# Kernel tuning notes

Measured on AMD Instinct MI355X. Metric: run time of the kernel, lower is better.

Reference implementation:

```python
import jax, jax.numpy as jnp
import numpy as np

D = 256       # video_dim == gcn_dims == interaction_dim
FD = 512      # forward_dim = 2 * interaction_dim
UPDATE_RATE = 0.5


def setup_inputs() -> dict:
    key = jax.random.key(0)
    ks = jax.random.split(key, 20)
    T, N = 768, 384
    s = lambda *sh: 1.0 / np.sqrt(sh[-1])
    return {
        "video_features": jax.random.normal(ks[0], (T, D), jnp.float32),
        "text_features": jax.random.normal(ks[1], (N, D), jnp.float32),
        "video_position_embedding": jax.random.normal(ks[2], (T, D), jnp.float32),
        "text_position_embedding": jax.random.normal(ks[3], (N, D), jnp.float32),
        # VideoEncoder conv1d (out=D, in=D, k=3)
        "conv_w": jax.random.normal(ks[4], (D, D, 3), jnp.float32) * (1.0 / np.sqrt(D * 3)),
        "conv_b": jax.random.normal(ks[5], (D,), jnp.float32) * 0.01,
        # TextGnnEncoder
        "bil_w": jax.random.normal(ks[6], (D, D), jnp.float32) * s(D, D),
        "lin_w": jax.random.normal(ks[7], (D, D), jnp.float32) * s(D, D),
        "lin_b": jax.random.normal(ks[8], (D,), jnp.float32) * 0.01,
        # PairInteraction
        "W1": jax.random.normal(ks[9], (FD, D), jnp.float32) * s(FD, D),
        "b1": jax.random.normal(ks[10], (FD,), jnp.float32) * 0.01,
        "W2": jax.random.normal(ks[11], (FD, D), jnp.float32) * s(FD, D),
        "Wi": jax.random.normal(ks[12], (D, FD), jnp.float32) * s(D, FD),
        "bi": jax.random.normal(ks[13], (D,), jnp.float32) * 0.01,
        # amplifier generators (Linear(interaction_dim, 1))
        "wt": jax.random.normal(ks[14], (D,), jnp.float32) * s(D,),
        "bt": jax.random.normal(ks[15], (1,), jnp.float32) * 0.01,
        "wv": jax.random.normal(ks[16], (D,), jnp.float32) * s(D,),
        "bv": jax.random.normal(ks[17], (1,), jnp.float32) * 0.01,
    }


def _forward(video_features, text_features, video_position_embedding, text_position_embedding,
             conv_w, conv_b, bil_w, lin_w, lin_b, W1, b1, W2, Wi, bi, wt, bt, wv, bv):
    T, N = video_features.shape[0], text_features.shape[0]
    input_video, input_text = video_features, text_features

    v = video_features + video_position_embedding          # (T, D)
    t = text_features + text_position_embedding            # (N, D)

    # VideoEncoder: Conv1d(k=3, pad=1) over time, then ReLU (dropout=0 in eval)
    x = v.T[None]                                           # (1, D, T)
    x = jax.lax.conv_general_dilated(x, conv_w, (1,), [(1, 1)],
                                     dimension_numbers=("NCH", "OIH", "NCH"))
    v = jax.nn.relu(x[0] + conv_b[:, None]).T               # (T, D)

    # TextGnnEncoder
    tn = t / jnp.maximum(jnp.linalg.norm(t, axis=1, keepdims=True), 1e-12)  # L2 normalize rows
    edges = (tn @ bil_w.T) @ tn.T                            # (N, N)
    weights = jax.nn.sigmoid(jnp.mean(edges, axis=1, keepdims=True))        # (N, 1)
    t = weights * (tn @ lin_w.T + lin_b)                     # (N, D)

    # PairInteraction: broadcast add + ReLU + Linear
    f1 = v @ W1.T + b1                                       # (T, FD)
    f2 = t @ W2.T                                            # (N, FD)
    h = jax.nn.relu(f1[:, None, :] + f2[None, :, :])         # (T, N, FD)
    imap = jnp.einsum("tnf,of->tno", h, Wi) + bi             # (T, N, D)

    # dual softmax attention pooling
    text_att = jax.nn.softmax(imap @ wt + bt, axis=1)        # (T, N), softmax over N
    text_context = jnp.einsum("tn,nd->td", text_att, t)      # (T, D)
    video_att = jax.nn.softmax(imap @ wv + bv, axis=0)       # (T, N), softmax over T
    video_context = jnp.einsum("tn,td->nd", video_att, v)    # (N, D)

    ur = UPDATE_RATE
    t_out = video_context * ur + t * (1.0 - ur) + input_text
    v_out = text_context * ur + v * (1.0 - ur) + input_video
    return v_out, t_out


def reference(video_features, text_features, video_position_embedding, text_position_embedding,
              conv_w, conv_b, bil_w, lin_w, lin_b, W1, b1, W2, Wi, bi, wt, bt, wv, bv):
    return _forward(video_features, text_features, video_position_embedding, text_position_embedding,
                    conv_w, conv_b, bil_w, lin_w, lin_b, W1, b1, W2, Wi, bi, wt, bt, wv, bv)
```

## Files before the change

### kernel.cpp

```cpp
#include <hip/hip_runtime.h>
#include <math.h>

#define D  256
#define T  768
#define N  384
#define FD 512

#define DOT4(A,B) ((A).x*(B).x + (A).y*(B).y + (A).z*(B).z + (A).w*(B).w)

__global__ __launch_bounds__(256) void k_front(
    const float* __restrict__ vf, const float* __restrict__ vpos,
    const float* __restrict__ cw,
    const float* __restrict__ tf, const float* __restrict__ tpos,
    const float* __restrict__ lin_w, const float* __restrict__ lin_b,
    const float* __restrict__ Wi, const float* __restrict__ wt,
    const float* __restrict__ wv,
    float* __restrict__ vep, float* __restrict__ tn,
    float* __restrict__ tl, float* __restrict__ ut, float* __restrict__ uv)
{
    __shared__ float smem[10880];
    const int b = blockIdx.x, tid = threadIdx.x;

    if (b < 288) {
        const int k  = b % 3;
        const int rem = b / 3;
        const int t0 = (rem % 12) * 64;
        const int o0 = (rem / 12) * 32;
        float (*As)[68] = (float(*)[68])smem;
        float (*Bs)[68] = (float(*)[68])(smem + 4352);
        const int p = tid >> 4, oi = tid & 15;
        float a00=0.f,a01=0.f,a10=0.f,a11=0.f,a20=0.f,a21=0.f,a30=0.f,a31=0.f;

        for (int c = 0; c < 4; ++c) {
            const int i0 = c << 6;
            __syncthreads();
#pragma unroll
            for (int s = 0; s < 4; ++s) {
                int u = tid + (s << 8);
                int r = u >> 4, q4 = (u & 15) * 4;
                int gr = t0 + r + k - 1;
                float4 v = make_float4(0.f,0.f,0.f,0.f);
                if (gr >= 0 && gr < T) {
                    float4 x = *(const float4*)&vf[gr*D + i0 + q4];
                    float4 y = *(const float4*)&vpos[gr*D + i0 + q4];
                    v = make_float4(x.x+y.x, x.y+y.y, x.z+y.z, x.w+y.w);
                }
                *(float4*)&As[r][q4] = v;
            }
#pragma unroll
            for (int s = 0; s < 8; ++s) {
                int u = tid + (s << 8);
                int o = u >> 6, i = u & 63;
                Bs[o][i] = cw[(o0 + o)*768 + (i0 + i)*3 + k];
            }
            __syncthreads();
#pragma unroll 4
            for (int kc4 = 0; kc4 < 16; ++kc4) {
                float4 r0 = *(const float4*)&As[4*p    ][kc4*4];
                float4 r1 = *(const float4*)&As[4*p + 1][kc4*4];
                float4 r2 = *(const float4*)&As[4*p + 2][kc4*4];
                float4 r3 = *(const float4*)&As[4*p + 3][kc4*4];
                float4 b0 = *(const float4*)&Bs[oi     ][kc4*4];
                float4 b1 = *(const float4*)&Bs[oi + 16][kc4*4];
                a00 += DOT4(r0,b0); a01 += DOT4(r0,b1);
                a10 += DOT4(r1,b0); a11 += DOT4(r1,b1);
                a20 += DOT4(r2,b0); a21 += DOT4(r2,b1);
                a30 += DOT4(r3,b0); a31 += DOT4(r3,b1);
            }
        }
        float* vz = vep + k * (T*D);
        const int t = t0 + 4*p;
        vz[(t  )*D + o0 + oi] = a00;  vz[(t  )*D + o0 + oi + 16] = a01;
        vz[(t+1)*D + o0 + oi] = a10;  vz[(t+1)*D + o0 + oi + 16] = a11;
        vz[(t+2)*D + o0 + oi] = a20;  vz[(t+2)*D + o0 + oi + 16] = a21;
        vz[(t+3)*D + o0 + oi] = a30;  vz[(t+3)*D + o0 + oi + 16] = a31;
    } else if (b < 384) {
        const int wid = tid >> 6, lane = tid & 63;
        const int r = (b - 288)*4 + wid;
        float v[4]; float ss = 0.f;
#pragma unroll
        for (int kk = 0; kk < 4; ++kk) {
            v[kk] = tf[r*D + lane + 64*kk] + tpos[r*D + lane + 64*kk];
            ss += v[kk]*v[kk];
        }
#pragma unroll
        for (int off = 1; off < 64; off <<= 1) ss += __shfl_xor(ss, off);
        float inv = 1.0f / fmaxf(sqrtf(ss), 1e-12f);
#pragma unroll
        for (int kk = 0; kk < 4; ++kk) tn[r*D + lane + 64*kk] = v[kk] * inv;
    } else if (b < 480) {
        const int bb = b - 384;
        const int n0 = (bb >> 3) * 32;
        const int o0 = (bb & 7) * 32;
        float (*As2)[260] = (float(*)[260])smem;
        float (*Bs2)[68]  = (float(*)[68])(smem + 8320);
        float* inv = smem + 10496;
#pragma unroll
        for (int s = 0; s < 8; ++s) {
            int u = tid + (s << 8);
            int r = u >> 6, q4 = (u & 63) * 4;
            float4 x = *(const float4*)&tf[(n0 + r)*D + q4];
            float4 y = *(const float4*)&tpos[(n0 + r)*D + q4];
            *(float4*)&As2[r][q4] = make_float4(x.x+y.x, x.y+y.y, x.z+y.z, x.w+y.w);
        }
        __syncthreads();
        {
            const int r = tid >> 3, j = tid & 7;
            float p = 0.f;
#pragma unroll
            for (int m = 0; m < 8; ++m) {
                float4 a = *(const float4*)&As2[r][j*32 + m*4];
                p += DOT4(a, a);
            }
            p += __shfl_xor(p, 1); p += __shfl_xor(p, 2); p += __shfl_xor(p, 4);
            if (j == 0) inv[r] = 1.0f / fmaxf(sqrtf(p), 1e-12f);
        }
        const int tA = tid >> 4, oA = tid & 15;
        float acc00=0.f, acc01=0.f, acc10=0.f, acc11=0.f;
        for (int c = 0; c < 4; ++c) {
            const int d0 = c << 6;
            __syncthreads();
#pragma unroll
            for (int s = 0; s < 2; ++s) {
                int u = tid + (s << 8);
                int o = u >> 4, q4 = (u & 15) * 4;
                *(float4*)&Bs2[o][q4] = *(const float4*)&lin_w[(o0 + o)*D + d0 + q4];
            }
            __syncthreads();
#pragma unroll 4
            for (int kc4 = 0; kc4 < 16; ++kc4) {
                float4 a0 = *(const float4*)&As2[tA     ][d0 + kc4*4];
                float4 a1 = *(const float4*)&As2[tA + 16][d0 + kc4*4];
                float4 b0 = *(const float4*)&Bs2[oA     ][kc4*4];
                float4 b1 = *(const float4*)&Bs2[oA + 16][kc4*4];
                acc00 += DOT4(a0,b0); acc01 += DOT4(a0,b1);
                acc10 += DOT4(a1,b0); acc11 += DOT4(a1,b1);
            }
        }
        const float i0n = inv[tA], i1n = inv[tA + 16];
        const float lb0 = lin_b[o0 + oA], lb1 = lin_b[o0 + oA + 16];
        tl[(n0 + tA     )*D + o0 + oA]      = i0n*acc00 + lb0;
        tl[(n0 + tA     )*D + o0 + oA + 16] = i0n*acc01 + lb1;
        tl[(n0 + tA + 16)*D + o0 + oA]      = i1n*acc10 + lb0;
        tl[(n0 + tA + 16)*D + o0 + oA + 16] = i1n*acc11 + lb1;
    } else {
        float* wsm = smem;
        const int which = b - 480;
        const float* w = (which < 2) ? wt : wv;
        float* u = (which < 2) ? ut : uv;
        const int f = ((which & 1) << 8) + tid;
        wsm[tid] = w[tid];
        __syncthreads();
        float s = 0.f;
#pragma unroll 4
        for (int d = 0; d < D; ++d) s += wsm[d] * Wi[d*FD + f];
        u[f] = s;
    }
}

__global__ __launch_bounds__(256) void k_mid(
    const float* __restrict__ vep, const float* __restrict__ cbp,
    const float* __restrict__ W1, const float* __restrict__ b1v,
    const float* __restrict__ tlp, const float* __restrict__ W2,
    const float* __restrict__ tn, const float* __restrict__ bil,
    float* __restrict__ f1, float* __restrict__ f2,
    float* __restrict__ ve, float* __restrict__ q)
{
    __shared__ float smem[6656];
    const int b = blockIdx.x, tid = threadIdx.x;

    if (b < 288) {
        const bool isF1 = (b < 192);
        const int bb = isF1 ? b : b - 192;
        const int nT = isF1 ? 12 : 6;
        const int r0 = (bb % nT) * 64;
        const int f0 = (bb / nT) * 32;
        float (*As)[68] = (float(*)[68])smem;
        float (*Bs)[68] = (float(*)[68])(smem + 4352);
        const int p = tid >> 4, fi = tid & 15;
        float a00=0.f,a01=0.f,a10=0.f,a11=0.f,a20=0.f,a21=0.f,a30=0.f,a31=0.f;
        const float* Wp = isF1 ? W1 : W2;

        for (int c = 0; c < 4; ++c) {
            const int d0 = c << 6;
            __syncthreads();
            if (isF1) {
#pragma unroll
                for (int s = 0; s < 4; ++s) {
                    int u = tid + (s << 8);
                    int r = u >> 4, q4 = (u & 15) * 4;
                    const int off = (r0 + r)*D + d0 + q4;
                    float4 p0 = *(const float4*)&vep[off];
                    float4 p1 = *(const float4*)&vep[T*D + off];
                    float4 p2 = *(const float4*)&vep[2*T*D + off];
                    float4 cbv = *(const float4*)&cbp[d0 + q4];
                    float4 v;
                    v.x = fmaxf(p0.x+p1.x+p2.x+cbv.x, 0.f);
                    v.y = fmaxf(p0.y+p1.y+p2.y+cbv.y, 0.f);
                    v.z = fmaxf(p0.z+p1.z+p2.z+cbv.z, 0.f);
                    v.w = fmaxf(p0.w+p1.w+p2.w+cbv.w, 0.f);
                    *(float4*)&As[r][q4] = v;
                }
            } else {
#pragma unroll
                for (int s = 0; s < 4; ++s) {
                    int u = tid + (s << 8);
                    int r = u >> 4, q4 = (u & 15) * 4;
                    *(float4*)&As[r][q4] = *(const float4*)&tlp[(r0 + r)*D + d0 + q4];
                }
            }
#pragma unroll
            for (int s = 0; s < 2; ++s) {
                int u = tid + (s << 8);
                int o = u >> 4, q4 = (u & 15) * 4;
                *(float4*)&Bs[o][q4] = *(const float4*)&Wp[(f0 + o)*D + d0 + q4];
            }
            __syncthreads();
#pragma unroll 4
            for (int kc4 = 0; kc4 < 16; ++kc4) {
                float4 r0v = *(const float4*)&As[4*p    ][kc4*4];
                float4 r1v = *(const float4*)&As[4*p + 1][kc4*4];
                float4 r2v = *(const float4*)&As[4*p + 2][kc4*4];
                float4 r3v = *(const float4*)&As[4*p + 3][kc4*4];
                float4 b0 = *(const float4*)&Bs[fi     ][kc4*4];
                float4 b1 = *(const float4*)&Bs[fi + 16][kc4*4];
                a00 += DOT4(r0v,b0); a01 += DOT4(r0v,b1);
                a10 += DOT4(r1v,b0); a11 += DOT4(r1v,b1);
                a20 += DOT4(r2v,b0); a21 += DOT4(r2v,b1);
                a30 += DOT4(r3v,b0); a31 += DOT4(r3v,b1);
            }
        }
        const int r = r0 + 4*p;
        if (isF1) {
            const float bi0 = b1v[f0 + fi], bi1 = b1v[f0 + fi + 16];
            f1[(r  )*FD + f0 + fi] = a00 + bi0;  f1[(r  )*FD + f0 + fi + 16] = a01 + bi1;
            f1[(r+1)*FD + f0 + fi] = a10 + bi0;  f1[(r+1)*FD + f0 + fi + 16] = a11 + bi1;
            f1[(r+2)*FD + f0 + fi] = a20 + bi0;  f1[(r+2)*FD + f0 + fi + 16] = a21 + bi1;
            f1[(r+3)*FD + f0 + fi] = a30 + bi0;  f1[(r+3)*FD + f0 + fi + 16] = a31 + bi1;
        } else {
            f2[(r  )*FD + f0 + fi] = a00;  f2[(r  )*FD + f0 + fi + 16] = a01;
            f2[(r+1)*FD + f0 + fi] = a10;  f2[(r+1)*FD + f0 + fi + 16] = a11;
            f2[(r+2)*FD + f0 + fi] = a20;  f2[(r+2)*FD + f0 + fi + 16] = a21;
            f2[(r+3)*FD + f0 + fi] = a30;  f2[(r+3)*FD + f0 + fi + 16] = a31;
        }
    } else if (b < 384) {
        const int t0 = (b - 288) * 8;
        float cbv = cbp[tid];
#pragma unroll
        for (int r = 0; r < 8; ++r) {
            const int off = (t0 + r)*D + tid;
            float s = vep[off] + vep[T*D + off] + vep[2*T*D + off] + cbv;
            ve[off] = fmaxf(s, 0.f);
        }
    } else {
        float* tb = smem;
        float (*qp)[32] = (float(*)[32])(smem + 256);
        const int bq = b - 384;
        float s = 0.f;
#pragma unroll 8
        for (int n = 0; n < N; ++n) s += tn[n*D + tid];
        tb[tid] = s * (1.0f / (float)N);
        __syncthreads();
        const int o = tid & 31, dg = tid >> 5;
        float p = 0.f;
#pragma unroll 8
        for (int d = dg*32; d < dg*32 + 32; ++d) p += tb[d] * bil[d*D + bq*32 + o];
        qp[dg][o] = p;
        __syncthreads();
        if (tid < 32) {
            float acc = 0.f;
#pragma unroll
            for (int kk = 0; kk < 8; ++kk) acc += qp[kk][tid];
            q[bq*32 + tid] = acc;
        }
    }
}

__global__ __launch_bounds__(256) void k_score(
    const float* __restrict__ f1, const float* __restrict__ f2,
    const float* __restrict__ tn, const float* __restrict__ qv,
    const float* __restrict__ tlp,
    const float* __restrict__ ut, const float* __restrict__ uv,
    float* __restrict__ stp, float* __restrict__ svp, float* __restrict__ tg)
{
    __shared__ float smem[9216];
    const int tid = threadIdx.x;
    const int bid = blockIdx.x;

    if (bid < 576) {
        const int t0 = (bid % 12) * 64;
        const int n0 = ((bid / 12) % 6) * 64;
        const int iz = bid / 72;
        const int fz = iz * 64;
        float (*f1s)[68] = (float(*)[68])smem;
        float (*f2s)[68] = (float(*)[68])(smem + 4352);
        float* qs   = smem + 8704;
        float* us_t = smem + 8960;
        float* us_v = smem + 9024;
        float* wsm  = smem + 9088;

        qs[tid] = qv[tid];
        if (tid < 64) us_t[tid] = ut[fz + tid];
        else if (tid < 128) us_v[tid - 64] = uv[fz + tid - 64];
        __syncthreads();
        {
            const int r = tid >> 2, j = tid & 3;
            float p = 0.f;
#pragma unroll
            for (int m = 0; m < 16; ++m) {
                float4 a = *(const float4*)&tn[(n0 + r)*D + j*64 + m*4];
                float4 qq = *(const float4*)&qs[j*64 + m*4];
                p += DOT4(a, qq);
            }
            p += __shfl_xor(p, 1); p += __shfl_xor(p, 2);
            if (j == 0) wsm[r] = 1.0f / (1.0f + expf(-p));
        }
#pragma unroll
        for (int s = 0; s < 4; ++s) {
            int u = tid + (s << 8);
            int r = u >> 4, q4 = (u & 15) * 4;
            *(float4*)&f1s[r][q4] = *(const float4*)&f1[(t0 + r)*FD + fz + q4];
        }
        __syncthreads();
#pragma unroll
        for (int s = 0; s < 4; ++s) {
            int u = tid + (s << 8);
            int r = u >> 4, q4 = (u & 15) * 4;
            float w = wsm[r];
            float4 v = *(const float4*)&f2[(n0 + r)*FD + fz + q4];
            *(float4*)&f2s[r][q4] = make_float4(w*v.x, w*v.y, w*v.z, w*v.w);
        }
        __syncthreads();

        const int ti = tid >> 4, ni = tid & 15;
        float at[4][4], av[4][4];
#pragma unroll
        for (int i = 0; i < 4; ++i)
#pragma unroll
            for (int j = 0; j < 4; ++j) { at[i][j] = 0.f; av[i][j] = 0.f; }

#pragma unroll 2
        for (int fq = 0; fq < 16; ++fq) {
            float a[4][4], bb[4][4], utv[4], uvv[4];
            *(float4*)utv  = *(const float4*)&us_t[fq*4];
            *(float4*)uvv  = *(const float4*)&us_v[fq*4];
#pragma unroll
            for (int i = 0; i < 4; ++i) {
                *(float4*)a[i]  = *(const float4*)&f1s[ti + 16*i][fq*4];
                *(float4*)bb[i] = *(const float4*)&f2s[ni + 16*i][fq*4];
            }
#pragma unroll
            for (int e = 0; e < 4; ++e) {
#pragma unroll
                for (int i = 0; i < 4; ++i) {
#pragma unroll
                    for (int j = 0; j < 4; ++j) {
                        float h = fmaxf(a[i][e] + bb[j][e], 0.f);
                        at[i][j] += h * utv[e];
                        av[i][j] += h * uvv[e];
                    }
                }
            }
        }
        float* stz = stp + iz * (T*N);
        float* svz = svp + iz * (N*T);
#pragma unroll
        for (int i = 0; i < 4; ++i) {
            const int t = t0 + ti + 16*i;
#pragma unroll
            for (int j = 0; j < 4; ++j) {
                const int n = n0 + ni + 16*j;
                stz[t*N + n] = at[i][j];
                svz[n*T + t] = av[i][j];
            }
        }
    } else {
        const int n0 = (bid - 576) * 32;
        float* qs  = smem;
        float* wsm = smem + 256;
        qs[tid] = qv[tid];
        __syncthreads();
        {
            const int r = tid >> 3, j = tid & 7;
            float p = 0.f;
#pragma unroll
            for (int m = 0; m < 8; ++m) {
                float4 a = *(const float4*)&tn[(n0 + r)*D + j*32 + m*4];
                float4 qq = *(const float4*)&qs[j*32 + m*4];
                p += DOT4(a, qq);
            }
            p += __shfl_xor(p, 1); p += __shfl_xor(p, 2); p += __shfl_xor(p, 4);
            if (j == 0) wsm[r] = 1.0f / (1.0f + expf(-p));
        }
        __syncthreads();
#pragma unroll
        for (int r = 0; r < 32; ++r)
            tg[(n0 + r)*D + tid] = wsm[r] * tlp[(n0 + r)*D + tid];
    }
}

__global__ __launch_bounds__(256) void k_att(
    const float* __restrict__ stp, const float* __restrict__ svp,
    const float* __restrict__ tg, const float* __restrict__ ve,
    const float* __restrict__ vf, const float* __restrict__ tf,
    float* __restrict__ out_v, float* __restrict__ out_t)
{
    __shared__ float attb[768][4];
    __shared__ float red[4][4];
    __shared__ float ptA[4][4][64];
    __shared__ float ptB[4][4][64];
    const int tid = threadIdx.x;
    const int oo = tid & 63, g = tid >> 6;
    const int TN = T*N;

    if (blockIdx.x < 384) {
        const int bx = blockIdx.x >> 1, h = blockIdx.x & 1;
        const int t0 = bx * 4;
        const int oA = h*128 + oo, oB = oA + 64;

        float v1[4], v2[4];
#pragma unroll
        for (int r = 0; r < 4; ++r) {
            const float* p = stp + (t0 + r)*N + tid;
            float s1 = 0.f;
#pragma unroll
            for (int z = 0; z < 8; ++z) s1 += p[z*TN];
            v1[r] = s1;
            if (tid < 128) {
                float s2 = 0.f;
#pragma unroll
                for (int z = 0; z < 8; ++z) s2 += p[z*TN + 256];
                v2[r] = s2;
            } else v2[r] = -1e30f;
        }
        float m[4], si[4];
#pragma unroll
        for (int r = 0; r < 4; ++r) {
            float mm = fmaxf(v1[r], v2[r]);
#pragma unroll
            for (int off = 1; off < 64; off <<= 1) mm = fmaxf(mm, __shfl_xor(mm, off));
            if (oo == 0) red[g][r] = mm;
        }
        __syncthreads();
#pragma unroll
        for (int r = 0; r < 4; ++r)
            m[r] = fmaxf(fmaxf(red[0][r], red[1][r]), fmaxf(red[2][r], red[3][r]));
        __syncthreads();
        float e1[4], e2[4];
#pragma unroll
        for (int r = 0; r < 4; ++r) {
            e1[r] = expf(v1[r] - m[r]);
            e2[r] = (tid < 128) ? expf(v2[r] - m[r]) : 0.f;
            float ss = e1[r] + e2[r];
#pragma unroll
            for (int off = 1; off < 64; off <<= 1) ss += __shfl_xor(ss, off);
            if (oo == 0) red[g][r] = ss;
        }
        __syncthreads();
#pragma unroll
        for (int r = 0; r < 4; ++r)
            si[r] = 1.0f / (red[0][r] + red[1][r] + red[2][r] + red[3][r]);
#pragma unroll
        for (int r = 0; r < 4; ++r) {
            attb[tid][r] = e1[r] * si[r];
            if (tid < 128) attb[tid + 256][r] = e2[r] * si[r];
        }
        __syncthreads();

        float accA[4] = {0.f,0.f,0.f,0.f};
        float accB[4] = {0.f,0.f,0.f,0.f};
#pragma unroll 4
        for (int n = g; n < N; n += 4) {
            float4 a0 = *(const float4*)&attb[n][0];
            float tvA = tg[n*D + oA], tvB = tg[n*D + oB];
            accA[0] += a0.x*tvA; accA[1] += a0.y*tvA; accA[2] += a0.z*tvA; accA[3] += a0.w*tvA;
            accB[0] += a0.x*tvB; accB[1] += a0.y*tvB; accB[2] += a0.z*tvB; accB[3] += a0.w*tvB;
        }
#pragma unroll
        for (int r = 0; r < 4; ++r) { ptA[g][r][oo] = accA[r]; ptB[g][r][oo] = accB[r]; }
        __syncthreads();
        if (g < 4) {
            const int rr = g;
            float sA = ptA[0][rr][oo] + ptA[1][rr][oo] + ptA[2][rr][oo] + ptA[3][rr][oo];
            float sB = ptB[0][rr][oo] + ptB[1][rr][oo] + ptB[2][rr][oo] + ptB[3][rr][oo];
            int t = t0 + rr;
            out_v[t*D + oA] = 0.5f*sA + 0.5f*ve[t*D + oA] + vf[t*D + oA];
            out_v[t*D + oB] = 0.5f*sB + 0.5f*ve[t*D + oB] + vf[t*D + oB];
        }
    } else {
        const int b2 = blockIdx.x - 384;
        const int bx = b2 >> 1, h = b2 & 1;
        const int n0 = bx * 4;
        const int oA = h*128 + oo, oB = oA + 64;

        float v1[4], v2[4], v3[4];
#pragma unroll
        for (int r = 0; r < 4; ++r) {
            const float* p = svp + (n0 + r)*T + tid;
            float s1 = 0.f, s2 = 0.f, s3 = 0.f;
#pragma unroll
            for (int z = 0; z < 8; ++z) {
                s1 += p[z*TN];
                s2 += p[z*TN + 256];
                s3 += p[z*TN + 512];
            }
            v1[r] = s1; v2[r] = s2; v3[r] = s3;
        }
        float m[4], si[4];
#pragma unroll
        for (int r = 0; r < 4; ++r) {
            float mm = fmaxf(fmaxf(v1[r], v2[r]), v3[r]);
#pragma unroll
            for (int off = 1; off < 64; off <<= 1) mm = fmaxf(mm, __shfl_xor(mm, off));
            if (oo == 0) red[g][r] = mm;
        }
        __syncthreads();
#pragma unroll
        for (int r = 0; r < 4; ++r)
            m[r] = fmaxf(fmaxf(red[0][r], red[1][r]), fmaxf(red[2][r], red[3][r]));
        __syncthreads();
        float e1[4], e2[4], e3[4];
#pragma unroll
        for (int r = 0; r < 4; ++r) {
            e1[r] = expf(v1[r] - m[r]);
            e2[r] = expf(v2[r] - m[r]);
            e3[r] = expf(v3[r] - m[r]);
            float ss = e1[r] + e2[r] + e3[r];
#pragma unroll
            for (int off = 1; off < 64; off <<= 1) ss += __shfl_xor(ss, off);
            if (oo == 0) red[g][r] = ss;
        }
        __syncthreads();
#pragma unroll
        for (int r = 0; r < 4; ++r)
            si[r] = 1.0f / (red[0][r] + red[1][r] + red[2][r] + red[3][r]);
#pragma unroll
        for (int r = 0; r < 4; ++r) {
            attb[tid][r]       = e1[r] * si[r];
            attb[tid + 256][r] = e2[r] * si[r];
            attb[tid + 512][r] = e3[r] * si[r];
        }
        __syncthreads();

        float accA[4] = {0.f,0.f,0.f,0.f};
        float accB[4] = {0.f,0.f,0.f,0.f};
#pragma unroll 4
        for (int t = g; t < T; t += 4) {
            float4 a0 = *(const float4*)&attb[t][0];
            float vvA = ve[t*D + oA], vvB = ve[t*D + oB];
            accA[0] += a0.x*vvA; accA[1] += a0.y*vvA; accA[2] += a0.z*vvA; accA[3] += a0.w*vvA;
            accB[0] += a0.x*vvB; accB[1] += a0.y*vvB; accB[2] += a0.z*vvB; accB[3] += a0.w*vvB;
        }
#pragma unroll
        for (int r = 0; r < 4; ++r) { ptA[g][r][oo] = accA[r]; ptB[g][r][oo] = accB[r]; }
        __syncthreads();
        if (g < 4) {
            const int rr = g;
            float sA = ptA[0][rr][oo] + ptA[1][rr][oo] + ptA[2][rr][oo] + ptA[3][rr][oo];
            float sB = ptB[0][rr][oo] + ptB[1][rr][oo] + ptB[2][rr][oo] + ptB[3][rr][oo];
            int n = n0 + rr;
            out_t[n*D + oA] = 0.5f*sA + 0.5f*tg[n*D + oA] + tf[n*D + oA];
            out_t[n*D + oB] = 0.5f*sB + 0.5f*tg[n*D + oB] + tf[n*D + oB];
        }
    }
}

extern "C" void kernel_launch(void* const* d_in, const int* in_sizes, int n_in,
                              void* d_out, int out_size, void* d_ws, size_t ws_size,
                              hipStream_t stream)
{
    (void)in_sizes; (void)n_in; (void)out_size; (void)ws_size;
    const float* vf   = (const float*)d_in[0];
    const float* tf   = (const float*)d_in[1];
    const float* vpos = (const float*)d_in[2];
    const float* tpos = (const float*)d_in[3];
    const float* cw   = (const float*)d_in[4];
    const float* cb   = (const float*)d_in[5];
    const float* bil  = (const float*)d_in[6];
    const float* lw   = (const float*)d_in[7];
    const float* lb   = (const float*)d_in[8];
    const float* W1   = (const float*)d_in[9];
    const float* b1   = (const float*)d_in[10];
    const float* W2   = (const float*)d_in[11];
    const float* Wi   = (const float*)d_in[12];
    const float* wt   = (const float*)d_in[14];
    const float* wv   = (const float*)d_in[16];

    float* ws  = (float*)d_ws;
    float* vep = ws;
    float* ve  = vep + 3*T*D;
    float* tn  = ve + T*D;
    float* tl  = tn + N*D;
    float* tg  = tl + N*D;
    float* f1  = tg + N*D;
    float* f2  = f1 + T*FD;
    float* q   = f2 + N*FD;
    float* ut  = q + D;
    float* uv  = ut + FD;
    float* stp = uv + FD;
    float* svp = stp + 8*T*N;

    float* out_v = (float*)d_out;
    float* out_t = out_v + T*D;

    hipLaunchKernelGGL(k_front, dim3(484), dim3(256), 0, stream,
                       vf, vpos, cw, tf, tpos, lw, lb, Wi, wt, wv, vep, tn, tl, ut, uv);
    hipLaunchKernelGGL(k_mid,   dim3(392), dim3(256), 0, stream,
                       vep, cb, W1, b1, tl, W2, tn, bil, f1, f2, ve, q);
    hipLaunchKernelGGL(k_score, dim3(588), dim3(256), 0, stream,
                       f1, f2, tn, q, tl, ut, uv, stp, svp, tg);
    hipLaunchKernelGGL(k_att,   dim3(576), dim3(256), 0, stream,
                       stp, svp, tg, ve, vf, tf, out_v, out_t);
}
```

Baseline: 99.22 us.

## Retile score kernel to 32x32 with fewer F-splits and coalesced stores; widen attention rows

The score kernel now uses 32x32 (t,n) tiles with the F dimension split two ways instead of eight, looping over four 64-wide F chunks inside the block. This cuts the partial-score buffers from 8 to 2 and so reduces the traffic that the attention kernel must read and sum. Results are staged through shared memory so both the row-major and transposed partial outputs are written as coalesced float4 stores. The attention kernel processes 8 rows per block instead of 4, halving its grid and reusing each loaded tg/ve value across more rows. In exchange each thread carries a smaller 2x2 register tile with less ILP, and both kernels now do more serial work per block on fewer blocks.

```diff
diff --git a/kernel.cpp b/kernel.cpp
--- a/kernel.cpp
+++ b/kernel.cpp
@@ -283,96 +283,93 @@
     const float* __restrict__ ut, const float* __restrict__ uv,
     float* __restrict__ stp, float* __restrict__ svp, float* __restrict__ tg)
 {
-    __shared__ float smem[9216];
+    __shared__ float smem[5152];
     const int tid = threadIdx.x;
     const int bid = blockIdx.x;
 
     if (bid < 576) {
-        const int t0 = (bid % 12) * 64;
-        const int n0 = ((bid / 12) % 6) * 64;
-        const int iz = bid / 72;
-        const int fz = iz * 64;
+        const int t0 = (bid % 24) * 32;
+        const int n0 = ((bid / 24) % 12) * 32;
+        const int iz = bid / 288;
+        const int fh = iz * 256;
         float (*f1s)[68] = (float(*)[68])smem;
-        float (*f2s)[68] = (float(*)[68])(smem + 4352);
-        float* qs   = smem + 8704;
-        float* us_t = smem + 8960;
-        float* us_v = smem + 9024;
-        float* wsm  = smem + 9088;
-
-        qs[tid] = qv[tid];
-        if (tid < 64) us_t[tid] = ut[fz + tid];
-        else if (tid < 128) us_v[tid - 64] = uv[fz + tid - 64];
+        float (*f2s)[68] = (float(*)[68])(smem + 2176);
+        float* us_t = smem + 4352;
+        float* us_v = smem + 4608;
+        float* qs   = smem + 4864;
+        float* wsm  = smem + 5120;
+
+        qs[tid]   = qv[tid];
+        us_t[tid] = ut[fh + tid];
+        us_v[tid] = uv[fh + tid];
         __syncthreads();
         {
-            const int r = tid >> 2, j = tid & 3;
+            const int r = tid >> 3, j = tid & 7;
             float p = 0.f;
 #pragma unroll
-            for (int m = 0; m < 16; ++m) {
-                float4 a = *(const float4*)&tn[(n0 + r)*D + j*64 + m*4];
-                float4 qq = *(const float4*)&qs[j*64 + m*4];
+            for (int m = 0; m < 8; ++m) {
+                float4 a = *(const float4*)&tn[(n0 + r)*D + j*32 + m*4];
+                float4 qq = *(const float4*)&qs[j*32 + m*4];
                 p += DOT4(a, qq);
             }
-            p += __shfl_xor(p, 1); p += __shfl_xor(p, 2);
+            p += __shfl_xor(p, 1); p += __shfl_xor(p, 2); p += __shfl_xor(p, 4);
             if (j == 0) wsm[r] = 1.0f / (1.0f + expf(-p));
         }
-#pragma unroll
-        for (int s = 0; s < 4; ++s) {
-            int u = tid + (s << 8);
-            int r = u >> 4, q4 = (u & 15) * 4;
-            *(float4*)&f1s[r][q4] = *(const float4*)&f1[(t0 + r)*FD + fz + q4];
-        }
-        __syncthreads();
-#pragma unroll
-        for (int s = 0; s < 4; ++s) {
-            int u = tid + (s << 8);
-            int r = u >> 4, q4 = (u & 15) * 4;
-            float w = wsm[r];
-            float4 v = *(const float4*)&f2[(n0 + r)*FD + fz + q4];
-            *(float4*)&f2s[r][q4] = make_float4(w*v.x, w*v.y, w*v.z, w*v.w);
-        }
-        __syncthreads();
 
         const int ti = tid >> 4, ni = tid & 15;
-        float at[4][4], av[4][4];
-#pragma unroll
-        for (int i = 0; i < 4; ++i)
-#pragma unroll
-            for (int j = 0; j < 4; ++j) { at[i][j] = 0.f; av[i][j] = 0.f; }
-
-#pragma unroll 2
-        for (int fq = 0; fq < 16; ++fq) {
-            float a[4][4], bb[4][4], utv[4], uvv[4];
-            *(float4*)utv  = *(const float4*)&us_t[fq*4];
-            *(float4*)uvv  = *(const float4*)&us_v[fq*4];
-#pragma unroll
-            for (int i = 0; i < 4; ++i) {
-                *(float4*)a[i]  = *(const float4*)&f1s[ti + 16*i][fq*4];
-                *(float4*)bb[i] = *(const float4*)&f2s[ni + 16*i][fq*4];
-            }
-#pragma unroll
-            for (int e = 0; e < 4; ++e) {
-#pragma unroll
-                for (int i = 0; i < 4; ++i) {
-#pragma unroll
-                    for (int j = 0; j < 4; ++j) {
-                        float h = fmaxf(a[i][e] + bb[j][e], 0.f);
-                        at[i][j] += h * utv[e];
-                        av[i][j] += h * uvv[e];
-                    }
+        float at[2][2] = {{0.f,0.f},{0.f,0.f}};
+        float av[2][2] = {{0.f,0.f},{0.f,0.f}};
+
+        for (int c = 0; c < 4; ++c) {
+            const int f00 = fh + c*64;
+            __syncthreads();
+#pragma unroll
+            for (int s = 0; s < 2; ++s) {
+                int u = tid + (s << 8);
+                int r = u >> 4, q4 = (u & 15) * 4;
+                *(float4*)&f1s[r][q4] = *(const float4*)&f1[(t0 + r)*FD + f00 + q4];
+                float w = wsm[r];
+                float4 v = *(const float4*)&f2[(n0 + r)*FD + f00 + q4];
+                *(float4*)&f2s[r][q4] = make_float4(w*v.x, w*v.y, w*v.z, w*v.w);
+            }
+            __syncthreads();
+#pragma unroll 4
+            for (int fq = 0; fq < 16; ++fq) {
+                float utv[4], uvv[4], a0[4], a1[4], b0[4], b1[4];
+                *(float4*)utv = *(const float4*)&us_t[c*64 + fq*4];
+                *(float4*)uvv = *(const float4*)&us_v[c*64 + fq*4];
+                *(float4*)a0  = *(const float4*)&f1s[ti     ][fq*4];
+                *(float4*)a1  = *(const float4*)&f1s[ti + 16][fq*4];
+                *(float4*)b0  = *(const float4*)&f2s[ni     ][fq*4];
+                *(float4*)b1  = *(const float4*)&f2s[ni + 16][fq*4];
+#pragma unroll
+                for (int e = 0; e < 4; ++e) {
+                    float h00 = fmaxf(a0[e] + b0[e], 0.f);
+                    float h01 = fmaxf(a0[e] + b1[e], 0.f);
+                    float h10 = fmaxf(a1[e] + b0[e], 0.f);
+                    float h11 = fmaxf(a1[e] + b1[e], 0.f);
+                    at[0][0] += h00*utv[e]; av[0][0] += h00*uvv[e];
+                    at[0][1] += h01*utv[e]; av[0][1] += h01*uvv[e];
+                    at[1][0] += h10*utv[e]; av[1][0] += h10*uvv[e];
+                    at[1][1] += h11*utv[e]; av[1][1] += h11*uvv[e];
                 }
             }
         }
+        __syncthreads();
+#pragma unroll
+        for (int i = 0; i < 2; ++i)
+#pragma unroll
+            for (int j = 0; j < 2; ++j) {
+                f1s[ti + 16*i][ni + 16*j] = at[i][j];
+                f2s[ni + 16*j][ti + 16*i] = av[i][j];
+            }
+        __syncthreads();
         float* stz = stp + iz * (T*N);
         float* svz = svp + iz * (N*T);
-#pragma unroll
-        for (int i = 0; i < 4; ++i) {
-            const int t = t0 + ti + 16*i;
-#pragma unroll
-            for (int j = 0; j < 4; ++j) {
-                const int n = n0 + ni + 16*j;
-                stz[t*N + n] = at[i][j];
-                svz[n*T + t] = av[i][j];
-            }
+        {
+            const int row = tid >> 3, c4 = (tid & 7) * 4;
+            *(float4*)&stz[(t0 + row)*N + n0 + c4] = *(const float4*)&f1s[row][c4];
+            *(float4*)&svz[(n0 + row)*T + t0 + c4] = *(const float4*)&f2s[row][c4];
         }
     } else {
         const int n0 = (bid - 576) * 32;
@@ -405,37 +402,29 @@
     const float* __restrict__ vf, const float* __restrict__ tf,
     float* __restrict__ out_v, float* __restrict__ out_t)
 {
-    __shared__ float attb[768][4];
-    __shared__ float red[4][4];
-    __shared__ float ptA[4][4][64];
-    __shared__ float ptB[4][4][64];
+    __shared__ float attb[768][8];
+    __shared__ float red[4][8];
+    __shared__ float ptA[4][8][64];
+    __shared__ float ptB[4][8][64];
     const int tid = threadIdx.x;
     const int oo = tid & 63, g = tid >> 6;
     const int TN = T*N;
 
-    if (blockIdx.x < 384) {
+    if (blockIdx.x < 192) {
         const int bx = blockIdx.x >> 1, h = blockIdx.x & 1;
-        const int t0 = bx * 4;
+        const int t0 = bx * 8;
         const int oA = h*128 + oo, oB = oA + 64;
 
-        float v1[4], v2[4];
-#pragma unroll
-        for (int r = 0; r < 4; ++r) {
+        float v1[8], v2[8];
+#pragma unroll
+        for (int r = 0; r < 8; ++r) {
             const float* p = stp + (t0 + r)*N + tid;
-            float s1 = 0.f;
-#pragma unroll
-            for (int z = 0; z < 8; ++z) s1 += p[z*TN];
-            v1[r] = s1;
-            if (tid < 128) {
-                float s2 = 0.f;
-#pragma unroll
-                for (int z = 0; z < 8; ++z) s2 += p[z*TN + 256];
-                v2[r] = s2;
-            } else v2[r] = -1e30f;
-        }
-        float m[4], si[4];
-#pragma unroll
-        for (int r = 0; r < 4; ++r) {
+            v1[r] = p[0] + p[TN];
+            v2[r] = (tid < 128) ? (p[256] + p[TN + 256]) : -1e30f;
+        }
+        float m[8], si[8];
+#pragma unroll
+        for (int r = 0; r < 8; ++r) {
             float mm = fmaxf(v1[r], v2[r]);
 #pragma unroll
             for (int off = 1; off < 64; off <<= 1) mm = fmaxf(mm, __shfl_xor(mm, off));
@@ -443,12 +432,12 @@
         }
         __syncthreads();
 #pragma unroll
-        for (int r = 0; r < 4; ++r)
+        for (int r = 0; r < 8; ++r)
             m[r] = fmaxf(fmaxf(red[0][r], red[1][r]), fmaxf(red[2][r], red[3][r]));
         __syncthreads();
-        float e1[4], e2[4];
-#pragma unroll
-        for (int r = 0; r < 4; ++r) {
+        float e1[8], e2[8];
+#pragma unroll
+        for (int r = 0; r < 8; ++r) {
             e1[r] = expf(v1[r] - m[r]);
             e2[r] = (tid < 128) ? expf(v2[r] - m[r]) : 0.f;
             float ss = e1[r] + e2[r];
@@ -458,29 +447,32 @@
         }
         __syncthreads();
 #pragma unroll
-        for (int r = 0; r < 4; ++r)
+        for (int r = 0; r < 8; ++r)
             si[r] = 1.0f / (red[0][r] + red[1][r] + red[2][r] + red[3][r]);
 #pragma unroll
-        for (int r = 0; r < 4; ++r) {
+        for (int r = 0; r < 8; ++r) {
             attb[tid][r] = e1[r] * si[r];
             if (tid < 128) attb[tid + 256][r] = e2[r] * si[r];
         }
         __syncthreads();
 
-        float accA[4] = {0.f,0.f,0.f,0.f};
-        float accB[4] = {0.f,0.f,0.f,0.f};
+        float accA[8] = {0.f,0.f,0.f,0.f,0.f,0.f,0.f,0.f};
+        float accB[8] = {0.f,0.f,0.f,0.f,0.f,0.f,0.f,0.f};
 #pragma unroll 4
         for (int n = g; n < N; n += 4) {
             float4 a0 = *(const float4*)&attb[n][0];
+            float4 a1 = *(const float4*)&attb[n][4];
             float tvA = tg[n*D + oA], tvB = tg[n*D + oB];
             accA[0] += a0.x*tvA; accA[1] += a0.y*tvA; accA[2] += a0.z*tvA; accA[3] += a0.w*tvA;
+            accA[4] += a1.x*tvA; accA[5] += a1.y*tvA; accA[6] += a1.z*tvA; accA[7] += a1.w*tvA;
             accB[0] += a0.x*tvB; accB[1] += a0.y*tvB; accB[2] += a0.z*tvB; accB[3] += a0.w*tvB;
-        }
-#pragma unroll
-        for (int r = 0; r < 4; ++r) { ptA[g][r][oo] = accA[r]; ptB[g][r][oo] = accB[r]; }
-        __syncthreads();
-        if (g < 4) {
-            const int rr = g;
+            accB[4] += a1.x*tvB; accB[5] += a1.y*tvB; accB[6] += a1.z*tvB; accB[7] += a1.w*tvB;
+        }
+#pragma unroll
+        for (int r = 0; r < 8; ++r) { ptA[g][r][oo] = accA[r]; ptB[g][r][oo] = accB[r]; }
+        __syncthreads();
+#pragma unroll
+        for (int rr = g; rr < 8; rr += 4) {
             float sA = ptA[0][rr][oo] + ptA[1][rr][oo] + ptA[2][rr][oo] + ptA[3][rr][oo];
             float sB = ptB[0][rr][oo] + ptB[1][rr][oo] + ptB[2][rr][oo] + ptB[3][rr][oo];
             int t = t0 + rr;
@@ -488,27 +480,22 @@
             out_v[t*D + oB] = 0.5f*sB + 0.5f*ve[t*D + oB] + vf[t*D + oB];
         }
     } else {
-        const int b2 = blockIdx.x - 384;
+        const int b2 = blockIdx.x - 192;
         const int bx = b2 >> 1, h = b2 & 1;
-        const int n0 = bx * 4;
+        const int n0 = bx * 8;
         const int oA = h*128 + oo, oB = oA + 64;
 
-        float v1[4], v2[4], v3[4];
-#pragma unroll
-        for (int r = 0; r < 4; ++r) {
+        float v1[8], v2[8], v3[8];
+#pragma unroll
+        for (int r = 0; r < 8; ++r) {
             const float* p = svp + (n0 + r)*T + tid;
-            float s1 = 0.f, s2 = 0.f, s3 = 0.f;
-#pragma unroll
-            for (int z = 0; z < 8; ++z) {
-                s1 += p[z*TN];
-                s2 += p[z*TN + 256];
-                s3 += p[z*TN + 512];
-            }
-            v1[r] = s1; v2[r] = s2; v3[r] = s3;
-        }
-        float m[4], si[4];
-#pragma unroll
-        for (int r = 0; r < 4; ++r) {
+            v1[r] = p[0]   + p[TN];
+            v2[r] = p[256] + p[TN + 256];
+            v3[r] = p[512] + p[TN + 512];
+        }
+        float m[8], si[8];
+#pragma unroll
+        for (int r = 0; r < 8; ++r) {
             float mm = fmaxf(fmaxf(v1[r], v2[r]), v3[r]);
 #pragma unroll
             for (int off = 1; off < 64; off <<= 1) mm = fmaxf(mm, __shfl_xor(mm, off));
@@ -516,12 +503,12 @@
         }
         __syncthreads();
 #pragma unroll
-        for (int r = 0; r < 4; ++r)
+        for (int r = 0; r < 8; ++r)
             m[r] = fmaxf(fmaxf(red[0][r], red[1][r]), fmaxf(red[2][r], red[3][r]));
         __syncthreads();
-        float e1[4], e2[4], e3[4];
-#pragma unroll
-        for (int r = 0; r < 4; ++r) {
+        float e1[8], e2[8], e3[8];
+#pragma unroll
+        for (int r = 0; r < 8; ++r) {
             e1[r] = expf(v1[r] - m[r]);
             e2[r] = expf(v2[r] - m[r]);
             e3[r] = expf(v3[r] - m[r]);
@@ -532,30 +519,33 @@
         }
         __syncthreads();
 #pragma unroll
-        for (int r = 0; r < 4; ++r)
+        for (int r = 0; r < 8; ++r)
             si[r] = 1.0f / (red[0][r] + red[1][r] + red[2][r] + red[3][r]);
 #pragma unroll
-        for (int r = 0; r < 4; ++r) {
+        for (int r = 0; r < 8; ++r) {
             attb[tid][r]       = e1[r] * si[r];
             attb[tid + 256][r] = e2[r] * si[r];
             attb[tid + 512][r] = e3[r] * si[r];
         }
         __syncthreads();
 
-        float accA[4] = {0.f,0.f,0.f,0.f};
-        float accB[4] = {0.f,0.f,0.f,0.f};
+        float accA[8] = {0.f,0.f,0.f,0.f,0.f,0.f,0.f,0.f};
+        float accB[8] = {0.f,0.f,0.f,0.f,0.f,0.f,0.f,0.f};
 #pragma unroll 4
         for (int t = g; t < T; t += 4) {
             float4 a0 = *(const float4*)&attb[t][0];
+            float4 a1 = *(const float4*)&attb[t][4];
             float vvA = ve[t*D + oA], vvB = ve[t*D + oB];
             accA[0] += a0.x*vvA; accA[1] += a0.y*vvA; accA[2] += a0.z*vvA; accA[3] += a0.w*vvA;
+            accA[4] += a1.x*vvA; accA[5] += a1.y*vvA; accA[6] += a1.z*vvA; accA[7] += a1.w*vvA;
             accB[0] += a0.x*vvB; accB[1] += a0.y*vvB; accB[2] += a0.z*vvB; accB[3] += a0.w*vvB;
-        }
-#pragma unroll
-        for (int r = 0; r < 4; ++r) { ptA[g][r][oo] = accA[r]; ptB[g][r][oo] = accB[r]; }
-        __syncthreads();
-        if (g < 4) {
-            const int rr = g;
+            accB[4] += a1.x*vvB; accB[5] += a1.y*vvB; accB[6] += a1.z*vvB; accB[7] += a1.w*vvB;
+        }
+#pragma unroll
+        for (int r = 0; r < 8; ++r) { ptA[g][r][oo] = accA[r]; ptB[g][r][oo] = accB[r]; }
+        __syncthreads();
+#pragma unroll
+        for (int rr = g; rr < 8; rr += 4) {
             float sA = ptA[0][rr][oo] + ptA[1][rr][oo] + ptA[2][rr][oo] + ptA[3][rr][oo];
             float sB = ptB[0][rr][oo] + ptB[1][rr][oo] + ptB[2][rr][oo] + ptB[3][rr][oo];
             int n = n0 + rr;
@@ -598,7 +588,7 @@
     float* ut  = q + D;
     float* uv  = ut + FD;
     float* stp = uv + FD;
-    float* svp = stp + 8*T*N;
+    float* svp = stp + 2*T*N;
 
     float* out_v = (float*)d_out;
     float* out_t = out_v + T*D;
@@ -609,6 +599,6 @@
                        vep, cb, W1, b1, tl, W2, tn, bil, f1, f2, ve, q);
     hipLaunchKernelGGL(k_score, dim3(588), dim3(256), 0, stream,
                        f1, f2, tn, q, tl, ut, uv, stp, svp, tg);
-    hipLaunchKernelGGL(k_att,   dim3(576), dim3(256), 0, stream,
+    hipLaunchKernelGGL(k_att,   dim3(288), dim3(256), 0, stream,
                        stp, svp, tg, ve, vf, tf, out_v, out_t);
 }
```

After: 99.88 us, median of 2. No clear change (+0.7%).
